# Kernel optimization log

Hardware: AMD Instinct MI355X
Metric: run time of the kernel (lower is better)

The kernel has to match this reference:

```python
import jax, jax.numpy as jnp
import numpy as np

B, S, D, H = 2, 2048, 1024, 16
HEAD_DIM = D // H
MAX_REL = 64  # max_relative_position in source


def setup_inputs() -> dict:
    key = jax.random.key(0)
    ks = jax.random.split(key, 8)
    std = 0.02
    return {
        "query": jax.random.normal(ks[0], (B, S, D), jnp.float32),
        "key": jax.random.normal(ks[1], (B, S, D), jnp.float32),
        "value": jax.random.normal(ks[2], (B, S, D), jnp.float32),
        "attention_mask": jnp.zeros((B, 1, 1, S), jnp.float32),
        "Wq": jax.random.normal(ks[3], (D, D), jnp.float32) * std,
        "bq": jnp.zeros((D,), jnp.float32),
        "Wk": jax.random.normal(ks[4], (D, D), jnp.float32) * std,
        "bk": jnp.zeros((D,), jnp.float32),
        "Wv": jax.random.normal(ks[5], (D, D), jnp.float32) * std,
        "bv": jnp.zeros((D,), jnp.float32),
        "rel_table": jax.random.normal(ks[6], (2 * MAX_REL + 1, HEAD_DIM), jnp.float32) * std,
    }


def _split_heads(x, b):
    # [B,S,D] -> [B,H,S,d]
    return x.reshape(b, -1, H, HEAD_DIM).transpose(0, 2, 1, 3)


def reference(query, key, value, attention_mask, Wq, bq, Wk, bk, Wv, bv, rel_table):
    b, s, _ = query.shape
    q = _split_heads(query @ Wq + bq, b)   # [B,H,S,d]
    k = _split_heads(key @ Wk + bk, b)
    v = _split_heads(value @ Wv + bv, b)

    scores = jnp.einsum("bhqd,bhkd->bhqk", q, k)  # [B,H,S,S]

    # relative-position key bias: rel_k[q_idx, k_idx] = table[clip(k-q)+MAX_REL]
    idx = jnp.arange(s)
    dist = jnp.clip(idx[None, :] - idx[:, None], -MAX_REL, MAX_REL) + MAX_REL  # [S,S]
    rel_k = rel_table[dist]  # [S,S,d]
    scores = scores + jnp.einsum("bhqd,qkd->bhqk", q, rel_k)

    scores = scores / jnp.sqrt(jnp.asarray(HEAD_DIM, scores.dtype))
    scores = scores + attention_mask  # additive mask, broadcast [B,1,1,S]

    probs = jax.nn.softmax(scores, axis=-1)  # dropout is identity (p=0 / eval)
    ctx = jnp.einsum("bhqk,bhkd->bhqd", probs, v)
    ctx = ctx.transpose(0, 2, 1, 3).reshape(b, s, H * HEAD_DIM)
    return ctx
```

## Files before the change

### kernel.cpp

```cpp
#include <hip/hip_runtime.h>
#include <hip/hip_bf16.h>

#define BB 2
#define SS 2048
#define DD 1024
#define HH 16
#define HD 64
#define NREL 129
#define LOG2E 1.4426950408889634f
#define SCALEQ (LOG2E / 8.0f)
#define KVB 131072l

typedef short s8v __attribute__((ext_vector_type(8)));
typedef short s4v __attribute__((ext_vector_type(4)));
typedef float f4 __attribute__((ext_vector_type(4)));

#define MFMA_BF16 __builtin_amdgcn_mfma_f32_16x16x32_bf16

__device__ __forceinline__ float bf2f(unsigned short u) {
  union { unsigned int i; float f; } x; x.i = ((unsigned int)u) << 16; return x.f;
}
__device__ __forceinline__ unsigned short f2bf(float f) {
  union { float f; unsigned int i; } x; x.f = f;
  unsigned int r = x.i + 0x7fffu + ((x.i >> 16) & 1u);
  return (unsigned short)(r >> 16);
}
__device__ __forceinline__ unsigned int pk2bf(float a, float b) {
  union { __hip_bfloat162 h2; unsigned int u; } c;
  c.h2 = __float22bfloat162_rn(float2{a, b});
  return c.u;
}
__device__ __forceinline__ void gl_lds16(const void* g, void* l) {
  __builtin_amdgcn_global_load_lds(
      (const __attribute__((address_space(1))) unsigned int*)g,
      (__attribute__((address_space(3))) unsigned int*)l, 16, 0, 0);
}

__global__ __launch_bounds__(256) void cvt_x(
    const float* __restrict__ xq, const float* __restrict__ xk,
    const float* __restrict__ xv, unsigned short* __restrict__ xb) {
  const int z = blockIdx.y;
  const float* in = (z == 0) ? xq : (z == 1) ? xk : xv;
  unsigned short* out = xb + (long)z * 4096 * DD;
  const long i = ((long)blockIdx.x * 256 + threadIdx.x) * 8;
  f4 a = *(const f4*)(in + i);
  f4 b = *(const f4*)(in + i + 4);
  unsigned int u[4];
  u[0] = pk2bf(a[0], a[1]); u[1] = pk2bf(a[2], a[3]);
  u[2] = pk2bf(b[0], b[1]); u[3] = pk2bf(b[2], b[3]);
  *(s8v*)(out + i) = *(s8v*)u;
}

__global__ __launch_bounds__(256) void cvt_w(
    const float* __restrict__ Wq, const float* __restrict__ Wk,
    const float* __restrict__ Wv, unsigned short* __restrict__ WTt) {
  __shared__ unsigned short tile[64][72];
  const int z = blockIdx.z;
  const float* in = (z == 0) ? Wq : (z == 1) ? Wk : Wv;
  unsigned short* out = WTt + (long)z * 1048576;
  const int c0 = blockIdx.x * 64, r0 = blockIdx.y * 64;
  const int t = threadIdx.x;
  const int r = t >> 2;
  #pragma unroll
  for (int j = 0; j < 4; ++j) {
    int cc = (t & 3) * 16 + j * 4;
    f4 v = *(const f4*)(in + (long)(r0 + r) * DD + c0 + cc);
    #pragma unroll
    for (int e = 0; e < 4; ++e) tile[r][cc + e] = f2bf(v[e]);
  }
  __syncthreads();
  const int c = t >> 2;
  #pragma unroll
  for (int h = 0; h < 2; ++h) {
    int r8 = (t & 3) + 4 * h;
    unsigned short vals[8];
    #pragma unroll
    for (int j = 0; j < 8; ++j) vals[j] = tile[r8 * 8 + j][c];
    int n = c0 + c, kb = r0 + r8 * 8;
    long off = ((long)(n >> 7) * 131072) + ((kb >> 6) * 8192) +
               (((kb & 63) >> 3) * 1024) + ((n & 127) * 8);
    *(s8v*)(out + off) = *(s8v*)vals;
  }
}

__global__ __launch_bounds__(256, 4) void proj_gemm(
    const unsigned short* __restrict__ Xb, const unsigned short* __restrict__ WTt,
    const float* __restrict__ bq, const float* __restrict__ bk,
    const float* __restrict__ bv,
    unsigned short* __restrict__ qbuf, unsigned short* __restrict__ ktile,
    unsigned short* __restrict__ vtile) {
  __shared__ __align__(16) unsigned short wt[8][128][8];
  unsigned short* wtf = &wt[0][0][0];
  const int z = blockIdx.z;
  const unsigned short* X = Xb + (long)z * 4096 * DD;
  const unsigned short* WTz = WTt + (long)z * 1048576;
  const float* bias = (z == 0) ? bq : (z == 1) ? bk : bv;

  const int n0 = blockIdx.x * 128, m0 = blockIdx.y * 128;
  const int t = threadIdx.x, w = t >> 6, l = t & 63;
  const int lm = l & 15, qd = l >> 4;

  f4 acc[8][2];
  #pragma unroll
  for (int i = 0; i < 8; ++i) { acc[i][0] = (f4)0.0f; acc[i][1] = (f4)0.0f; }

  const unsigned short* x0 = X + (long)(m0 + w * 32 + lm) * DD;
  const unsigned short* x1 = x0 + 16 * DD;
  const unsigned short* wtile0 = WTz + (long)(n0 >> 7) * 131072;

  for (int k0 = 0; k0 < DD; k0 += 64) {
    __syncthreads();
    const unsigned short* tb = wtile0 + (k0 >> 6) * 8192;
    #pragma unroll
    for (int i = 0; i < 4; ++i) {
      int idx = w * 4 + i;
      gl_lds16(tb + idx * 512 + l * 8, wtf + idx * 512);
    }
    s8v a00 = *(const s8v*)(x0 + k0 + qd * 8);
    s8v a01 = *(const s8v*)(x0 + k0 + 32 + qd * 8);
    s8v a10 = *(const s8v*)(x1 + k0 + qd * 8);
    s8v a11 = *(const s8v*)(x1 + k0 + 32 + qd * 8);
    asm volatile("s_waitcnt vmcnt(0)" ::: "memory");
    __syncthreads();
    #pragma unroll
    for (int cb = 0; cb < 8; ++cb) {
      s8v b0 = *(const s8v*)&wt[qd][cb * 16 + lm][0];
      s8v b1 = *(const s8v*)&wt[4 + qd][cb * 16 + lm][0];
      acc[cb][0] = MFMA_BF16(a00, b0, acc[cb][0], 0, 0, 0);
      acc[cb][0] = MFMA_BF16(a01, b1, acc[cb][0], 0, 0, 0);
      acc[cb][1] = MFMA_BF16(a10, b0, acc[cb][1], 0, 0, 0);
      acc[cb][1] = MFMA_BF16(a11, b1, acc[cb][1], 0, 0, 0);
    }
  }
  if (z == 0) {
    #pragma unroll
    for (int cb = 0; cb < 8; ++cb) {
      int n = n0 + cb * 16 + lm;
      float bvv = bias[n];
      int hh = n >> 6, d = n & 63;
      #pragma unroll
      for (int ms = 0; ms < 2; ++ms) {
        #pragma unroll
        for (int r = 0; r < 4; ++r) {
          int m = m0 + w * 32 + ms * 16 + qd * 4 + r;
          int bidx = m >> 11, s = m & (SS - 1);
          qbuf[((long)(bidx * HH + hh) * SS + s) * HD + d] =
              f2bf((acc[cb][ms][r] + bvv) * SCALEQ);
        }
      }
    }
  } else if (z == 1) {
    #pragma unroll
    for (int cb = 0; cb < 8; ++cb) {
      int n = n0 + cb * 16 + lm;
      float bvv = bias[n];
      int hh = n >> 6, d = n & 63;
      int c = d >> 3, e = d & 7;
      #pragma unroll
      for (int ms = 0; ms < 2; ++ms) {
        #pragma unroll
        for (int r = 0; r < 4; ++r) {
          int m = m0 + w * 32 + ms * 16 + qd * 4 + r;
          int bidx = m >> 11, s = m & (SS - 1);
          long bh = bidx * HH + hh;
          ktile[bh * KVB + (s >> 6) * 4096 + c * 512 + (s & 63) * 8 + e] =
              f2bf(acc[cb][ms][r] + bvv);
        }
      }
    }
  } else {
    #pragma unroll
    for (int cb = 0; cb < 8; ++cb) {
      int n = n0 + cb * 16 + lm;
      float bvv = bias[n];
      int hh = n >> 6, d = n & 63;
      #pragma unroll
      for (int ms = 0; ms < 2; ++ms) {
        int m = m0 + w * 32 + ms * 16 + qd * 4;
        int bidx = m >> 11, s = m & (SS - 1);
        long bh = bidx * HH + hh;
        unsigned short o4[4];
        #pragma unroll
        for (int r = 0; r < 4; ++r) o4[r] = f2bf(acc[cb][ms][r] + bvv);
        *(s4v*)&vtile[bh * KVB + (s >> 6) * 4096 + ((s & 63) >> 3) * 512 +
                      d * 8 + (s & 7)] = *(s4v*)o4;
      }
    }
  }
}

__global__ __launch_bounds__(256, 2) void attn(
    const unsigned short* __restrict__ qb, const unsigned short* __restrict__ ktile,
    const unsigned short* __restrict__ vtile, const float* __restrict__ tableF,
    const float* __restrict__ maskF, float* __restrict__ out) {
  __shared__ __align__(16) unsigned short ks[2][8][64][8];
  __shared__ __align__(16) unsigned short vs[2][8][64][8];
  __shared__ __align__(16) unsigned short qr2[NREL][130];
  __shared__ __align__(16) unsigned short pbuf[4][16][40];
  __shared__ float mk[SS];

  const int bh = blockIdx.y, b = bh >> 4, h = bh & 15;
  const int q0 = blockIdx.x * 128;
  const int t = threadIdx.x, w = t >> 6, l = t & 63;
  const int lm = l & 15, qd = l >> 4;
  const int qw = q0 + w * 32;
  const int qc0 = w * 32 + lm, qc1 = qc0 + 16;

  const unsigned short* kkb = ktile + (long)bh * KVB;
  const unsigned short* vvb = vtile + (long)bh * KVB;

  #pragma unroll
  for (int i = 0; i < 2; ++i) {
    int c = 2 * w + i;
    gl_lds16(kkb + c * 512 + l * 8, &ks[0][c][0][0]);
    gl_lds16(vvb + c * 512 + l * 8, &vs[0][c][0][0]);
  }

  {
    const float* mrow = maskF + b * SS;
    f4 m0v = *(const f4*)(mrow + t * 8);
    f4 m1v = *(const f4*)(mrow + t * 8 + 4);
    #pragma unroll
    for (int e = 0; e < 4; ++e) {
      mk[t * 8 + e] = m0v[e] * LOG2E;
      mk[t * 8 + 4 + e] = m1v[e] * LOG2E;
    }
  }

  const unsigned short* qrow = qb + ((long)bh * SS + qw + lm) * HD;
  const s8v qa0 = *(const s8v*)(qrow + qd * 8);
  const s8v qa1 = *(const s8v*)(qrow + 32 + qd * 8);
  const s8v qb0 = *(const s8v*)(qrow + 16 * HD + qd * 8);
  const s8v qb1 = *(const s8v*)(qrow + 16 * HD + 32 + qd * 8);

  #pragma unroll
  for (int cb = 0; cb < 9; ++cb) {
    int dist = cb * 16 + lm;
    int dc = dist > NREL - 1 ? NREL - 1 : dist;
    const float* trow = tableF + dc * HD;
    f4 t0 = *(const f4*)(trow + qd * 8);
    f4 t1 = *(const f4*)(trow + qd * 8 + 4);
    f4 t2 = *(const f4*)(trow + 32 + qd * 8);
    f4 t3 = *(const f4*)(trow + 32 + qd * 8 + 4);
    unsigned int tb[8];
    tb[0] = pk2bf(t0[0], t0[1]); tb[1] = pk2bf(t0[2], t0[3]);
    tb[2] = pk2bf(t1[0], t1[1]); tb[3] = pk2bf(t1[2], t1[3]);
    tb[4] = pk2bf(t2[0], t2[1]); tb[5] = pk2bf(t2[2], t2[3]);
    tb[6] = pk2bf(t3[0], t3[1]); tb[7] = pk2bf(t3[2], t3[3]);
    s8v b0 = *(s8v*)tb, b1 = *(s8v*)(tb + 4);
    f4 c0 = MFMA_BF16(qa0, b0, (f4)0.0f, 0, 0, 0);
    c0 = MFMA_BF16(qa1, b1, c0, 0, 0, 0);
    f4 c1 = MFMA_BF16(qb0, b0, (f4)0.0f, 0, 0, 0);
    c1 = MFMA_BF16(qb1, b1, c1, 0, 0, 0);
    if (dist <= NREL - 1) {
      #pragma unroll
      for (int r = 0; r < 4; ++r) {
        qr2[dist][w * 32 + qd * 4 + r] = f2bf(c0[r]);
        qr2[dist][w * 32 + 16 + qd * 4 + r] = f2bf(c1[r]);
      }
    }
  }
  asm volatile("s_waitcnt vmcnt(0)" ::: "memory");
  __syncthreads();

  const float bLo0 = bf2f(qr2[0][qc0]), bHi0 = bf2f(qr2[128][qc0]);
  const float bLo1 = bf2f(qr2[0][qc1]), bHi1 = bf2f(qr2[128][qc1]);

  float m0_ = -1e30f, l0_ = 0.0f, m1_ = -1e30f, l1_ = 0.0f;
  f4 c40[4], c41[4];
  #pragma unroll
  for (int i = 0; i < 4; ++i) { c40[i] = (f4)0.0f; c41[i] = (f4)0.0f; }

  for (int rr = 0; rr < 32; ++rr) {
    const int kk = rr << 6;
    const int buf = rr & 1;
    if (rr < 31) {
      const int nb = buf ^ 1;
      const unsigned short* kg = kkb + (rr + 1) * 4096;
      const unsigned short* vg = vvb + (rr + 1) * 4096;
      #pragma unroll
      for (int i = 0; i < 2; ++i) {
        int c = 2 * w + i;
        gl_lds16(kg + c * 512 + l * 8, &ks[nb][c][0][0]);
        gl_lds16(vg + c * 512 + l * 8, &vs[nb][c][0][0]);
      }
    }
    f4 st0[4], st1[4];
    #pragma unroll
    for (int tt = 0; tt < 4; ++tt) {
      s8v k0v = *(const s8v*)&ks[buf][qd][tt * 16 + lm][0];
      s8v k1v = *(const s8v*)&ks[buf][4 + qd][tt * 16 + lm][0];
      st0[tt] = MFMA_BF16(k0v, qa0, (f4)0.0f, 0, 0, 0);
      st0[tt] = MFMA_BF16(k1v, qa1, st0[tt], 0, 0, 0);
      st1[tt] = MFMA_BF16(k0v, qb0, (f4)0.0f, 0, 0, 0);
      st1[tt] = MFMA_BF16(k1v, qb1, st1[tt], 0, 0, 0);
    }
    float z0[16], z1[16];
    const int kw = kk - qw;
    if (kw >= 96) {
      #pragma unroll
      for (int tt = 0; tt < 4; ++tt) {
        f4 mv = *(const f4*)&mk[kk + tt * 16 + qd * 4];
        #pragma unroll
        for (int r = 0; r < 4; ++r) {
          z0[tt * 4 + r] = st0[tt][r] + bHi0 + mv[r];
          z1[tt * 4 + r] = st1[tt][r] + bHi1 + mv[r];
        }
      }
    } else if (kw <= -128) {
      #pragma unroll
      for (int tt = 0; tt < 4; ++tt) {
        f4 mv = *(const f4*)&mk[kk + tt * 16 + qd * 4];
        #pragma unroll
        for (int r = 0; r < 4; ++r) {
          z0[tt * 4 + r] = st0[tt][r] + bLo0 + mv[r];
          z1[tt * 4 + r] = st1[tt][r] + bLo1 + mv[r];
        }
      }
    } else {
      const int db0 = kw - lm + 64 + qd * 4;
      #pragma unroll
      for (int tt = 0; tt < 4; ++tt) {
        f4 mv = *(const f4*)&mk[kk + tt * 16 + qd * 4];
        #pragma unroll
        for (int r = 0; r < 4; ++r) {
          int du = db0 + tt * 16 + r;
          int d0 = du < 0 ? 0 : (du > 128 ? 128 : du);
          int d1 = du - 16; d1 = d1 < 0 ? 0 : (d1 > 128 ? 128 : d1);
          z0[tt * 4 + r] = st0[tt][r] + bf2f(qr2[d0][qc0]) + mv[r];
          z1[tt * 4 + r] = st1[tt][r] + bf2f(qr2[d1][qc1]) + mv[r];
        }
      }
    }
    float tm0 = z0[0], tm1 = z1[0];
    #pragma unroll
    for (int i = 1; i < 16; ++i) {
      tm0 = fmaxf(tm0, z0[i]);
      tm1 = fmaxf(tm1, z1[i]);
    }
    tm0 = fmaxf(tm0, __shfl_xor(tm0, 16));
    tm0 = fmaxf(tm0, __shfl_xor(tm0, 32));
    tm1 = fmaxf(tm1, __shfl_xor(tm1, 16));
    tm1 = fmaxf(tm1, __shfl_xor(tm1, 32));
    float mn0 = fmaxf(m0_, tm0), mn1 = fmaxf(m1_, tm1);
    float al0 = __builtin_amdgcn_exp2f(m0_ - mn0);
    float al1 = __builtin_amdgcn_exp2f(m1_ - mn1);
    m0_ = mn0; m1_ = mn1;
    float s0 = 0.0f, s1 = 0.0f;
    #pragma unroll
    for (int i = 0; i < 16; ++i) {
      z0[i] = __builtin_amdgcn_exp2f(z0[i] - mn0); s0 += z0[i];
      z1[i] = __builtin_amdgcn_exp2f(z1[i] - mn1); s1 += z1[i];
    }
    s0 += __shfl_xor(s0, 16);
    s0 += __shfl_xor(s0, 32);
    s1 += __shfl_xor(s1, 16);
    s1 += __shfl_xor(s1, 32);
    l0_ = l0_ * al0 + s0; l1_ = l1_ * al1 + s1;
    #pragma unroll
    for (int db = 0; db < 4; ++db)
      #pragma unroll
      for (int r = 0; r < 4; ++r) { c40[db][r] *= al0; c41[db][r] *= al1; }

    {
      s8v va[4];
      #pragma unroll
      for (int db = 0; db < 4; ++db)
        va[db] = *(const s8v*)&vs[buf][qd][db * 16 + lm][0];
      *(unsigned int*)&pbuf[w][lm][qd * 4] = pk2bf(z0[0], z0[1]);
      *(unsigned int*)&pbuf[w][lm][qd * 4 + 2] = pk2bf(z0[2], z0[3]);
      *(unsigned int*)&pbuf[w][lm][16 + qd * 4] = pk2bf(z0[4], z0[5]);
      *(unsigned int*)&pbuf[w][lm][16 + qd * 4 + 2] = pk2bf(z0[6], z0[7]);
      asm volatile("s_waitcnt lgkmcnt(0)" ::: "memory");
      {
        s8v pa = *(const s8v*)&pbuf[w][lm][qd * 8];
        #pragma unroll
        for (int db = 0; db < 4; ++db)
          c40[db] = MFMA_BF16(va[db], pa, c40[db], 0, 0, 0);
      }
      *(unsigned int*)&pbuf[w][lm][qd * 4] = pk2bf(z1[0], z1[1]);
      *(unsigned int*)&pbuf[w][lm][qd * 4 + 2] = pk2bf(z1[2], z1[3]);
      *(unsigned int*)&pbuf[w][lm][16 + qd * 4] = pk2bf(z1[4], z1[5]);
      *(unsigned int*)&pbuf[w][lm][16 + qd * 4 + 2] = pk2bf(z1[6], z1[7]);
      asm volatile("s_waitcnt lgkmcnt(0)" ::: "memory");
      {
        s8v pa = *(const s8v*)&pbuf[w][lm][qd * 8];
        #pragma unroll
        for (int db = 0; db < 4; ++db)
          c41[db] = MFMA_BF16(va[db], pa, c41[db], 0, 0, 0);
      }
    }
    {
      s8v vb[4];
      #pragma unroll
      for (int db = 0; db < 4; ++db)
        vb[db] = *(const s8v*)&vs[buf][4 + qd][db * 16 + lm][0];
      *(unsigned int*)&pbuf[w][lm][qd * 4] = pk2bf(z0[8], z0[9]);
      *(unsigned int*)&pbuf[w][lm][qd * 4 + 2] = pk2bf(z0[10], z0[11]);
      *(unsigned int*)&pbuf[w][lm][16 + qd * 4] = pk2bf(z0[12], z0[13]);
      *(unsigned int*)&pbuf[w][lm][16 + qd * 4 + 2] = pk2bf(z0[14], z0[15]);
      asm volatile("s_waitcnt lgkmcnt(0)" ::: "memory");
      {
        s8v pb = *(const s8v*)&pbuf[w][lm][qd * 8];
        #pragma unroll
        for (int db = 0; db < 4; ++db)
          c40[db] = MFMA_BF16(vb[db], pb, c40[db], 0, 0, 0);
      }
      *(unsigned int*)&pbuf[w][lm][qd * 4] = pk2bf(z1[8], z1[9]);
      *(unsigned int*)&pbuf[w][lm][qd * 4 + 2] = pk2bf(z1[10], z1[11]);
      *(unsigned int*)&pbuf[w][lm][16 + qd * 4] = pk2bf(z1[12], z1[13]);
      *(unsigned int*)&pbuf[w][lm][16 + qd * 4 + 2] = pk2bf(z1[14], z1[15]);
      asm volatile("s_waitcnt lgkmcnt(0)" ::: "memory");
      {
        s8v pb = *(const s8v*)&pbuf[w][lm][qd * 8];
        #pragma unroll
        for (int db = 0; db < 4; ++db)
          c41[db] = MFMA_BF16(vb[db], pb, c41[db], 0, 0, 0);
      }
    }
    asm volatile("s_waitcnt vmcnt(0)" ::: "memory");
    __syncthreads();
  }

  const float inv0 = 1.0f / l0_, inv1 = 1.0f / l1_;
  float* ob0 = out + ((long)b * SS + q0 + qc0) * DD + h * HD;
  float* ob1 = out + ((long)b * SS + q0 + qc1) * DD + h * HD;
  #pragma unroll
  for (int db = 0; db < 4; ++db) {
    f4 o0, o1;
    #pragma unroll
    for (int r = 0; r < 4; ++r) {
      o0[r] = c40[db][r] * inv0;
      o1[r] = c41[db][r] * inv1;
    }
    *(f4*)(ob0 + db * 16 + qd * 4) = o0;
    *(f4*)(ob1 + db * 16 + qd * 4) = o1;
  }
}

extern "C" void kernel_launch(void* const* d_in, const int* in_sizes, int n_in,
                              void* d_out, int out_size, void* d_ws, size_t ws_size,
                              hipStream_t stream) {
  const float* query = (const float*)d_in[0];
  const float* key   = (const float*)d_in[1];
  const float* value = (const float*)d_in[2];
  const float* mask  = (const float*)d_in[3];
  const float* Wq    = (const float*)d_in[4];
  const float* bq    = (const float*)d_in[5];
  const float* Wk    = (const float*)d_in[6];
  const float* bk    = (const float*)d_in[7];
  const float* Wv    = (const float*)d_in[8];
  const float* bv    = (const float*)d_in[9];
  const float* table = (const float*)d_in[10];

  char* ws = (char*)d_ws;
  unsigned short* WTt   = (unsigned short*)(ws);
  unsigned short* Xb    = (unsigned short*)(ws + (8l << 20));
  unsigned short* qbuf  = (unsigned short*)(ws + (32l << 20));
  unsigned short* ktile = (unsigned short*)(ws + (40l << 20));
  unsigned short* vtile = (unsigned short*)(ws + (48l << 20));

  cvt_x<<<dim3(2048, 3, 1), 256, 0, stream>>>(query, key, value, Xb);

  cvt_w<<<dim3(16, 16, 3), 256, 0, stream>>>(Wq, Wk, Wv, WTt);

  proj_gemm<<<dim3(8, 32, 3), 256, 0, stream>>>(Xb, WTt, bq, bk, bv,
                                                qbuf, ktile, vtile);

  attn<<<dim3(16, 32, 1), 256, 0, stream>>>(qbuf, ktile, vtile, table, mask,
                                            (float*)d_out);
}
```

Before: 234.9 us.

## Move rel-bias and mask tables from LDS to global scratch to raise occupancy

The per-block q·rel_table product table (129×128 bf16) and the scaled mask row are moved out of shared memory. The mask is pre-scaled by the conversion kernel into a global buffer, and the relative-bias values go to a per-block global scratch that reuses the Xb region. This shrinks LDS use so launch bounds can request 4 blocks per CU instead of 2. In exchange, the inner-loop bias gathers and mask reads now hit global memory and rely on cache, and the kernel depends on global writes being visible to other threads after a __syncthreads.

```diff
diff --git a/kernel.cpp b/kernel.cpp
--- a/kernel.cpp
+++ b/kernel.cpp
@@ -7,6 +7,7 @@
 #define HH 16
 #define HD 64
 #define NREL 129
+#define QRS 132
 #define LOG2E 1.4426950408889634f
 #define SCALEQ (LOG2E / 8.0f)
 #define KVB 131072l
@@ -38,7 +39,8 @@
 
 __global__ __launch_bounds__(256) void cvt_x(
     const float* __restrict__ xq, const float* __restrict__ xk,
-    const float* __restrict__ xv, unsigned short* __restrict__ xb) {
+    const float* __restrict__ xv, const float* __restrict__ mask,
+    unsigned short* __restrict__ xb, float* __restrict__ mkg) {
   const int z = blockIdx.y;
   const float* in = (z == 0) ? xq : (z == 1) ? xk : xv;
   unsigned short* out = xb + (long)z * 4096 * DD;
@@ -49,6 +51,17 @@
   u[0] = pk2bf(a[0], a[1]); u[1] = pk2bf(a[2], a[3]);
   u[2] = pk2bf(b[0], b[1]); u[3] = pk2bf(b[2], b[3]);
   *(s8v*)(out + i) = *(s8v*)u;
+  if (z == 0 && blockIdx.x < BB) {
+    const int row = blockIdx.x;
+    const long j = (long)row * SS + threadIdx.x * 8;
+    f4 ma = *(const f4*)(mask + j);
+    f4 mb = *(const f4*)(mask + j + 4);
+    #pragma unroll
+    for (int e = 0; e < 4; ++e) {
+      mkg[j + e] = ma[e] * LOG2E;
+      mkg[j + 4 + e] = mb[e] * LOG2E;
+    }
+  }
 }
 
 __global__ __launch_bounds__(256) void cvt_w(
@@ -189,15 +202,14 @@
   }
 }
 
-__global__ __launch_bounds__(256, 2) void attn(
+__global__ __launch_bounds__(256, 4) void attn(
     const unsigned short* __restrict__ qb, const unsigned short* __restrict__ ktile,
     const unsigned short* __restrict__ vtile, const float* __restrict__ tableF,
-    const float* __restrict__ maskF, float* __restrict__ out) {
+    const float* __restrict__ mkg, unsigned short* __restrict__ qrg,
+    float* __restrict__ out) {
   __shared__ __align__(16) unsigned short ks[2][8][64][8];
   __shared__ __align__(16) unsigned short vs[2][8][64][8];
-  __shared__ __align__(16) unsigned short qr2[NREL][130];
   __shared__ __align__(16) unsigned short pbuf[4][16][40];
-  __shared__ float mk[SS];
 
   const int bh = blockIdx.y, b = bh >> 4, h = bh & 15;
   const int q0 = blockIdx.x * 128;
@@ -208,23 +220,13 @@
 
   const unsigned short* kkb = ktile + (long)bh * KVB;
   const unsigned short* vvb = vtile + (long)bh * KVB;
+  unsigned short* qblk = qrg + ((long)(bh * 16 + blockIdx.x)) * 128 * QRS;
 
   #pragma unroll
   for (int i = 0; i < 2; ++i) {
     int c = 2 * w + i;
     gl_lds16(kkb + c * 512 + l * 8, &ks[0][c][0][0]);
     gl_lds16(vvb + c * 512 + l * 8, &vs[0][c][0][0]);
-  }
-
-  {
-    const float* mrow = maskF + b * SS;
-    f4 m0v = *(const f4*)(mrow + t * 8);
-    f4 m1v = *(const f4*)(mrow + t * 8 + 4);
-    #pragma unroll
-    for (int e = 0; e < 4; ++e) {
-      mk[t * 8 + e] = m0v[e] * LOG2E;
-      mk[t * 8 + 4 + e] = m1v[e] * LOG2E;
-    }
   }
 
   const unsigned short* qrow = qb + ((long)bh * SS + qw + lm) * HD;
@@ -255,16 +257,19 @@
     if (dist <= NREL - 1) {
       #pragma unroll
       for (int r = 0; r < 4; ++r) {
-        qr2[dist][w * 32 + qd * 4 + r] = f2bf(c0[r]);
-        qr2[dist][w * 32 + 16 + qd * 4 + r] = f2bf(c1[r]);
+        qblk[(w * 32 + qd * 4 + r) * QRS + dist] = f2bf(c0[r]);
+        qblk[(w * 32 + 16 + qd * 4 + r) * QRS + dist] = f2bf(c1[r]);
       }
     }
   }
   asm volatile("s_waitcnt vmcnt(0)" ::: "memory");
   __syncthreads();
 
-  const float bLo0 = bf2f(qr2[0][qc0]), bHi0 = bf2f(qr2[128][qc0]);
-  const float bLo1 = bf2f(qr2[0][qc1]), bHi1 = bf2f(qr2[128][qc1]);
+  const unsigned short* qr0 = qblk + qc0 * QRS;
+  const unsigned short* qr1 = qblk + qc1 * QRS;
+  const float bLo0 = bf2f(qr0[0]), bHi0 = bf2f(qr0[128]);
+  const float bLo1 = bf2f(qr1[0]), bHi1 = bf2f(qr1[128]);
+  const float* mrow = mkg + b * SS;
 
   float m0_ = -1e30f, l0_ = 0.0f, m1_ = -1e30f, l1_ = 0.0f;
   f4 c40[4], c41[4];
@@ -300,7 +305,7 @@
     if (kw >= 96) {
       #pragma unroll
       for (int tt = 0; tt < 4; ++tt) {
-        f4 mv = *(const f4*)&mk[kk + tt * 16 + qd * 4];
+        f4 mv = *(const f4*)&mrow[kk + tt * 16 + qd * 4];
         #pragma unroll
         for (int r = 0; r < 4; ++r) {
           z0[tt * 4 + r] = st0[tt][r] + bHi0 + mv[r];
@@ -310,7 +315,7 @@
     } else if (kw <= -128) {
       #pragma unroll
       for (int tt = 0; tt < 4; ++tt) {
-        f4 mv = *(const f4*)&mk[kk + tt * 16 + qd * 4];
+        f4 mv = *(const f4*)&mrow[kk + tt * 16 + qd * 4];
         #pragma unroll
         for (int r = 0; r < 4; ++r) {
           z0[tt * 4 + r] = st0[tt][r] + bLo0 + mv[r];
@@ -321,14 +326,14 @@
       const int db0 = kw - lm + 64 + qd * 4;
       #pragma unroll
       for (int tt = 0; tt < 4; ++tt) {
-        f4 mv = *(const f4*)&mk[kk + tt * 16 + qd * 4];
+        f4 mv = *(const f4*)&mrow[kk + tt * 16 + qd * 4];
         #pragma unroll
         for (int r = 0; r < 4; ++r) {
           int du = db0 + tt * 16 + r;
           int d0 = du < 0 ? 0 : (du > 128 ? 128 : du);
           int d1 = du - 16; d1 = d1 < 0 ? 0 : (d1 > 128 ? 128 : d1);
-          z0[tt * 4 + r] = st0[tt][r] + bf2f(qr2[d0][qc0]) + mv[r];
-          z1[tt * 4 + r] = st1[tt][r] + bf2f(qr2[d1][qc1]) + mv[r];
+          z0[tt * 4 + r] = st0[tt][r] + bf2f(qr0[d0]) + mv[r];
+          z1[tt * 4 + r] = st1[tt][r] + bf2f(qr1[d1]) + mv[r];
         }
       }
     }
@@ -455,18 +460,20 @@
 
   char* ws = (char*)d_ws;
   unsigned short* WTt   = (unsigned short*)(ws);
+  float*          mkg   = (float*)(ws + (7l << 20));
   unsigned short* Xb    = (unsigned short*)(ws + (8l << 20));
+  unsigned short* qrg   = (unsigned short*)(ws + (8l << 20));
   unsigned short* qbuf  = (unsigned short*)(ws + (32l << 20));
   unsigned short* ktile = (unsigned short*)(ws + (40l << 20));
   unsigned short* vtile = (unsigned short*)(ws + (48l << 20));
 
-  cvt_x<<<dim3(2048, 3, 1), 256, 0, stream>>>(query, key, value, Xb);
+  cvt_x<<<dim3(2048, 3, 1), 256, 0, stream>>>(query, key, value, mask, Xb, mkg);
 
   cvt_w<<<dim3(16, 16, 3), 256, 0, stream>>>(Wq, Wk, Wv, WTt);
 
   proj_gemm<<<dim3(8, 32, 3), 256, 0, stream>>>(Xb, WTt, bq, bk, bv,
                                                 qbuf, ktile, vtile);
 
-  attn<<<dim3(16, 32, 1), 256, 0, stream>>>(qbuf, ktile, vtile, table, mask,
-                                            (float*)d_out);
-}
+  attn<<<dim3(16, 32, 1), 256, 0, stream>>>(qbuf, ktile, vtile, table,
+                                            mkg, qrg, (float*)d_out);
+}
```

New measurement: 427.7 us. +82.1%, slower.
